# Optimization experiments

Hardware: AMD Instinct MI355X
Metric: run time of the kernel (lower is better)

Reference implementation:

```python
import jax, jax.numpy as jnp
import numpy as np

TEMP = 1.0  # routing_temperature

def _gelu(x):
    return jax.nn.gelu(x, approximate=False)  # torch nn.GELU default (erf)

def setup_inputs() -> dict:
    key = jax.random.key(0)
    ks = jax.random.split(key, 6)
    B, S, D, E, I = 8, 2048, 768, 8, 3072
    H = I // 2
    def xav(k, shape):
        fan_in, fan_out = shape[-2], shape[-1]
        lim = float(np.sqrt(6.0 / (fan_in + fan_out)))
        return jax.random.uniform(k, shape, jnp.float32, -lim, lim)
    return {
        "x":  jax.random.normal(ks[0], (B, S, D), jnp.float32),
        "Wr": xav(ks[1], (D, E)),
        "br": jnp.zeros((E,), jnp.float32),
        "W1": xav(ks[2], (E, D, I)), "b1": jnp.zeros((E, I), jnp.float32),
        "W2": xav(ks[3], (E, I, H)), "b2": jnp.zeros((E, H), jnp.float32),
        "W3": xav(ks[4], (E, H, D)), "b3": jnp.zeros((E, D), jnp.float32),
        "top_k": 2,
    }

def reference(x, Wr, br, W1, b1, W2, b2, W3, b3, top_k):
    B, S, D = x.shape
    E = Wr.shape[1]
    T = B * S
    xt = x.reshape(T, D)                              # flatten tokens
    logits = (xt @ Wr + br) / TEMP                    # [T, E]
    vals, sel = jax.lax.top_k(logits, top_k)          # [T, k]
    w = jax.nn.softmax(vals, axis=-1)                 # softmax over top-k scores
    # dense per-token combine weights (zero for unselected experts)
    combine = jnp.zeros((T, E), x.dtype).at[jnp.arange(T)[:, None], sel].add(w)
    def step(acc, p):
        W1e, b1e, W2e, b2e, W3e, b3e, ce = p
        h = _gelu(xt @ W1e + b1e)                     # [T, I]
        h = _gelu(h @ W2e + b2e)                      # [T, I//2]
        y = h @ W3e + b3e                             # [T, D]
        return acc + ce[:, None] * y, None
    acc0 = jnp.zeros((T, D), x.dtype)
    out, _ = jax.lax.scan(step, acc0, (W1, b1, W2, b2, W3, b3, combine.T))
    return out.reshape(B, S, D)
```

## Files before the change

kernel.cpp:

```cpp
#include <hip/hip_runtime.h>
#include <hip/hip_fp16.h>
#include <cstdint>
#include <cstddef>

#define TK 16384
#define DD 768
#define EE 8
#define II 3072
#define HH 1536

typedef _Float16 half8 __attribute__((ext_vector_type(8)));
typedef float floatx4 __attribute__((ext_vector_type(4)));

typedef const __attribute__((address_space(1))) uint32_t* gptr_t;
typedef __attribute__((address_space(3))) uint32_t* lptr_t;

#define GLOAD_LDS16(gp, lp) __builtin_amdgcn_global_load_lds( \
    (gptr_t)(const void*)(gp), (lptr_t)(void*)(lp), 16, 0, 0)

__device__ __forceinline__ void xcd_swizzle(int& e, int& m, int& n, bool rev) {
  int gx = gridDim.x, gy = gridDim.y;
  int f = (blockIdx.z * gy + blockIdx.y) * gx + blockIdx.x;
  if (rev) f = gx * gy * 8 - 1 - f;
  int xcd = f & 7, idx = f >> 3;
  int chunk = idx / gx, pos = idx - chunk * gx;
  int logical = chunk * (8 * gx) + xcd * gx + pos;
  int mn = gy * gx;
  e = logical / mn;
  int rem = logical - e * mn;
  m = rem / gx;
  n = rem - m * gx;
}

__global__ __launch_bounds__(256)
void cvtT_kernel(const float* __restrict__ in, __half* __restrict__ out,
                 int K, int N) {
  __shared__ float tile[64][65];
  int e = blockIdx.z;
  const float* inp = in + (size_t)e * K * N + (size_t)(blockIdx.y * 64) * N + blockIdx.x * 64;
  __half* outp = out + (size_t)e * K * N + (size_t)(blockIdx.x * 64) * K + blockIdx.y * 64;
  int s = threadIdx.x;
  int tx = s & 15, r0 = s >> 4;
#pragma unroll
  for (int i = 0; i < 4; ++i) {
    int k = r0 + i * 16;
    float4 v = *(const float4*)&inp[(size_t)k * N + tx * 4];
    tile[k][tx * 4 + 0] = v.x;
    tile[k][tx * 4 + 1] = v.y;
    tile[k][tx * 4 + 2] = v.z;
    tile[k][tx * 4 + 3] = v.w;
  }
  __syncthreads();
  int kp = s & 31;
#pragma unroll
  for (int i = 0; i < 8; ++i) {
    int n = (s >> 5) + i * 8;
    __half2 h = __floats2half2_rn(tile[2 * kp][n], tile[2 * kp + 1][n]);
    *(__half2*)&outp[(size_t)n * K + kp * 2] = h;
  }
}

__global__ __launch_bounds__(256)
void router_kernel(const float* __restrict__ x, const float* __restrict__ Wr,
                   const float* __restrict__ br, int* __restrict__ counts,
                   int* __restrict__ sel, float* __restrict__ wTok,
                   __half* __restrict__ xh) {
  __shared__ float wr_s[EE * DD];
  for (int i = threadIdx.x; i < EE * DD; i += 256) {
    int d = i >> 3, e = i & 7;
    wr_s[e * DD + d] = Wr[i];
  }
  __syncthreads();
  int wid = threadIdx.x >> 6, lane = threadIdx.x & 63;
  int t = blockIdx.x * 4 + wid;
  const float* xt = x + (size_t)t * DD;
  float acc[EE];
#pragma unroll
  for (int e = 0; e < EE; ++e) acc[e] = 0.f;
  for (int d = lane; d < DD; d += 64) {
    float xv = xt[d];
#pragma unroll
    for (int e = 0; e < EE; ++e) acc[e] += xv * wr_s[e * DD + d];
  }
#pragma unroll
  for (int off = 32; off > 0; off >>= 1)
#pragma unroll
    for (int e = 0; e < EE; ++e) acc[e] += __shfl_xor(acc[e], off);
  if (lane == 0) {
    float v[EE];
#pragma unroll
    for (int e = 0; e < EE; ++e) v[e] = acc[e] + br[e];
    int i0 = 0;
#pragma unroll
    for (int e = 1; e < EE; ++e) if (v[e] > v[i0]) i0 = e;
    int i1 = (i0 == 0) ? 1 : 0;
#pragma unroll
    for (int e = 0; e < EE; ++e) if (e != i0 && v[e] > v[i1] && e != i1) { if (v[e] > v[i1]) i1 = e; }
    float e1 = __expf(v[i1] - v[i0]);
    float s = 1.f / (1.f + e1);
    sel[2 * t] = i0; sel[2 * t + 1] = i1;
    wTok[2 * t] = s; wTok[2 * t + 1] = e1 * s;
    atomicAdd(&counts[i0], 1);
    atomicAdd(&counts[i1], 1);
  }
  const float4* xr = (const float4*)xt;
  uint2* xo = (uint2*)(xh + (size_t)t * DD);
#pragma unroll
  for (int j = 0; j < 3; ++j) {
    float4 v = xr[lane + j * 64];
    __half2 a = __floats2half2_rn(v.x, v.y);
    __half2 b = __floats2half2_rn(v.z, v.w);
    uint2 p;
    p.x = *(const unsigned int*)&a;
    p.y = *(const unsigned int*)&b;
    xo[lane + j * 64] = p;
  }
}

__global__ void offsets_kernel(const int* __restrict__ counts, int* __restrict__ offsets,
                               int* __restrict__ cursors) {
  if (threadIdx.x == 0) {
    int o = 0;
    for (int e = 0; e < EE; ++e) { offsets[e] = o; cursors[e] = o; o += counts[e]; }
  }
}

__global__ void scatter_kernel(const int* __restrict__ sel, int* __restrict__ cursors,
                               int* __restrict__ idxList, int* __restrict__ posTok) {
  int t = blockIdx.x * 256 + threadIdx.x;
  if (t < TK) {
#pragma unroll
    for (int k = 0; k < 2; ++k) {
      int e = sel[2 * t + k];
      int p = atomicAdd(&cursors[e], 1);
      idxList[p] = t;
      posTok[2 * t + k] = p;
    }
  }
}

template<int KD, int ND, bool GATHER, bool GELU, bool REV>
__device__ __forceinline__
void ffn_body(const __half* __restrict__ A, const __half* __restrict__ Wt,
              const float* __restrict__ Bias, __half* __restrict__ Out,
              const int* __restrict__ counts, const int* __restrict__ offsets,
              const int* __restrict__ idxList) {
  constexpr int NT = KD / 32;
  int e, mblk, nblk;
  xcd_swizzle(e, mblk, nblk, REV);
  const int cnt = counts[e];
  const int m0 = mblk * 256;
  if (cnt == 0 || m0 >= cnt) return;
  const int off = offsets[e];
  const int n0 = nblk * 256;
  const __half* We = Wt + (size_t)e * KD * ND;
  const float* be = Bias + (size_t)e * ND;

  __shared__ __align__(16) __half AsF[5 * 256 * 32];
  __shared__ __align__(16) __half BsF[4 * 256 * 32];

  const int tid = threadIdx.x;
  const int colh = (((tid & 3) ^ ((tid >> 3) & 3)) << 3);
  const __half* aptr2[2];
  const __half* bptr2[2];
#pragma unroll
  for (int i = 0; i < 2; ++i) {
    int r = i * 128 + (tid >> 2);
    int gr = m0 + r; if (gr > cnt - 1) gr = cnt - 1;
    size_t arow = GATHER ? (size_t)idxList[off + gr] : (size_t)(off + gr);
    aptr2[i] = A + arow * KD + colh;
    bptr2[i] = We + (size_t)(n0 + r) * KD + colh;
  }

#define STA(WOFF, TS) do { \
    GLOAD_LDS16(aptr2[0] + (TS) * 32, (char*)AsF + (WOFF) + tid * 16); \
    GLOAD_LDS16(aptr2[1] + (TS) * 32, (char*)AsF + (WOFF) + tid * 16 + 8192); } while (0)
#define STB(WOFF, TS) do { \
    GLOAD_LDS16(bptr2[0] + (TS) * 32, (char*)BsF + (WOFF) + tid * 16); \
    GLOAD_LDS16(bptr2[1] + (TS) * 32, (char*)BsF + (WOFF) + tid * 16 + 8192); } while (0)

  const int lane = tid & 63, wv = tid >> 6;
  const int wr = wv >> 2, wc = wv & 3;
  const int lrow = lane & 15, lg = lane >> 4;
  const int slotSwz = lg ^ ((lrow >> 1) & 3);
  const int aBase = (wr * 128 + lrow) * 64 + slotSwz * 16;
  const int bBase = (wc * 64 + lrow) * 64 + slotSwz * 16;

  floatx4 acc[8][4];
#pragma unroll
  for (int mi = 0; mi < 8; ++mi)
#pragma unroll
    for (int ni = 0; ni < 4; ++ni) acc[mi][ni] = (floatx4){0.f, 0.f, 0.f, 0.f};

  STA(0 * 16384, 0);
  STB(0 * 16384, 0);
  STA(1 * 16384, 1);
  STB(1 * 16384, 1);
  STA(2 * 16384, 2);
  STB(2 * 16384, 2);
  STA(3 * 16384, 3);
  asm volatile("s_waitcnt vmcnt(10)" ::: "memory");
  __builtin_amdgcn_s_barrier();
  __builtin_amdgcn_sched_barrier(0);

  int rA = 0, wA = 4 * 16384;
  int rB = 0, wB = 3 * 16384;

#pragma unroll 1
  for (int t = 0; t < NT; ++t) {
    half8 af[8], bf[4];
#pragma unroll
    for (int mi = 0; mi < 8; ++mi)
      af[mi] = *(const half8*)((const char*)AsF + rA + aBase + mi * 1024);
#pragma unroll
    for (int ni = 0; ni < 4; ++ni)
      bf[ni] = *(const half8*)((const char*)BsF + rB + bBase + ni * 1024);
    if (t + 3 < NT) STB(wB, t + 3);
    if (t + 4 < NT) STA(wA, t + 4);
    __builtin_amdgcn_s_setprio(1);
#pragma unroll
    for (int mi = 0; mi < 8; ++mi)
#pragma unroll
      for (int ni = 0; ni < 4; ++ni)
        acc[mi][ni] = __builtin_amdgcn_mfma_f32_16x16x32_f16(
            af[mi], bf[ni], acc[mi][ni], 0, 0, 0);
    __builtin_amdgcn_s_setprio(0);
    if (t + 4 < NT) { asm volatile("s_waitcnt vmcnt(10)" ::: "memory"); }
    else            { asm volatile("s_waitcnt vmcnt(0)"  ::: "memory"); }
    __builtin_amdgcn_s_barrier();
    __builtin_amdgcn_sched_barrier(0);
    rA += 16384; if (rA == 5 * 16384) rA = 0;
    wA += 16384; if (wA == 5 * 16384) wA = 0;
    rB += 16384; if (rB == 4 * 16384) rB = 0;
    wB += 16384; if (wB == 4 * 16384) wB = 0;
  }

  const int crow = m0 + wr * 128 + lg * 4;
  const int ccol = n0 + wc * 64 + lrow;
  float bv[4];
#pragma unroll
  for (int ni = 0; ni < 4; ++ni) bv[ni] = be[ccol + ni * 16];
#pragma unroll
  for (int mi = 0; mi < 8; ++mi) {
#pragma unroll
    for (int j = 0; j < 4; ++j) {
      int r = crow + mi * 16 + j;
      if (r < cnt) {
#pragma unroll
        for (int ni = 0; ni < 4; ++ni) {
          float v = acc[mi][ni][j] + bv[ni];
          if (GELU) v = 0.5f * v * (1.f + erff(v * 0.70710678118654752f));
          Out[(size_t)(off + r) * ND + ccol + ni * 16] = __float2half(v);
        }
      }
    }
  }
#undef STA
#undef STB
}

__global__ __launch_bounds__(512, 1)
void ffn_s1(const __half* __restrict__ A, const __half* __restrict__ Wt,
            const float* __restrict__ Bias, __half* __restrict__ Out,
            const int* __restrict__ counts, const int* __restrict__ offsets,
            const int* __restrict__ idxL) {
  ffn_body<DD, II, true, true, false>(A, Wt, Bias, Out, counts, offsets, idxL);
}
__global__ __launch_bounds__(512, 1)
void ffn_s2(const __half* __restrict__ A, const __half* __restrict__ Wt,
            const float* __restrict__ Bias, __half* __restrict__ Out,
            const int* __restrict__ counts, const int* __restrict__ offsets,
            const int* __restrict__ idxL) {
  ffn_body<II, HH, false, true, true>(A, Wt, Bias, Out, counts, offsets, idxL);
}
__global__ __launch_bounds__(512, 1)
void ffn_s3(const __half* __restrict__ A, const __half* __restrict__ Wt,
            const float* __restrict__ Bias, __half* __restrict__ Out,
            const int* __restrict__ counts, const int* __restrict__ offsets,
            const int* __restrict__ idxL) {
  ffn_body<HH, DD, false, false, false>(A, Wt, Bias, Out, counts, offsets, idxL);
}

__global__ void combine_kernel(const __half* __restrict__ yc, const float* __restrict__ wTok,
                               const int* __restrict__ posTok, float* __restrict__ out) {
  int t = blockIdx.x;
  int d = threadIdx.x * 4;
  if (d >= DD) return;
  float w0 = wTok[2 * t], w1 = wTok[2 * t + 1];
  const __half2* a = (const __half2*)(yc + (size_t)posTok[2 * t] * DD + d);
  const __half2* b = (const __half2*)(yc + (size_t)posTok[2 * t + 1] * DD + d);
  float2 a0 = __half22float2(a[0]), a1 = __half22float2(a[1]);
  float2 b0 = __half22float2(b[0]), b1 = __half22float2(b[1]);
  float4 r;
  r.x = w0 * a0.x + w1 * b0.x;
  r.y = w0 * a0.y + w1 * b0.y;
  r.z = w0 * a1.x + w1 * b1.x;
  r.w = w0 * a1.y + w1 * b1.y;
  *(float4*)(out + (size_t)t * DD + d) = r;
}

extern "C" void kernel_launch(void* const* d_in, const int* in_sizes, int n_in,
                              void* d_out, int out_size, void* d_ws, size_t ws_size,
                              hipStream_t stream) {
  const float* x  = (const float*)d_in[0];
  const float* Wr = (const float*)d_in[1];
  const float* br = (const float*)d_in[2];
  const float* W1 = (const float*)d_in[3];
  const float* b1 = (const float*)d_in[4];
  const float* W2 = (const float*)d_in[5];
  const float* b2 = (const float*)d_in[6];
  const float* W3 = (const float*)d_in[7];
  const float* b3 = (const float*)d_in[8];
  float* out = (float*)d_out;

  char* ws = (char*)d_ws;
  size_t o = 0;
  auto alloc = [&](size_t bytes) {
    char* p = ws + o;
    o += (bytes + 255) & ~(size_t)255;
    return p;
  };
  __half* xh   = (__half*)alloc((size_t)TK * DD * 2);
  __half* w1t  = (__half*)alloc((size_t)EE * DD * II * 2);
  __half* w2t  = (__half*)alloc((size_t)EE * II * HH * 2);
  __half* w3t  = (__half*)alloc((size_t)EE * HH * DD * 2);
  __half* h1   = (__half*)alloc((size_t)2 * TK * II * 2);
  __half* h2   = (__half*)alloc((size_t)2 * TK * HH * 2);
  __half* yc   = (__half*)alloc((size_t)2 * TK * DD * 2);
  int*   idxL  = (int*)alloc(2 * TK * 4);
  int*   sel   = (int*)alloc(2 * TK * 4);
  float* wTok  = (float*)alloc(2 * TK * 4);
  int*   posT  = (int*)alloc(2 * TK * 4);
  int*   counts  = (int*)alloc(256);
  int*   offsets = (int*)alloc(256);
  int*   cursors = (int*)alloc(256);
  if (o > ws_size) return;

  hipMemsetAsync(counts, 0, 256, stream);

  cvtT_kernel<<<dim3(II / 64, DD / 64, EE), 256, 0, stream>>>(W1, w1t, DD, II);
  cvtT_kernel<<<dim3(HH / 64, II / 64, EE), 256, 0, stream>>>(W2, w2t, II, HH);
  cvtT_kernel<<<dim3(DD / 64, HH / 64, EE), 256, 0, stream>>>(W3, w3t, HH, DD);
  router_kernel<<<TK / 4, 256, 0, stream>>>(x, Wr, br, counts, sel, wTok, xh);
  offsets_kernel<<<1, 64, 0, stream>>>(counts, offsets, cursors);
  scatter_kernel<<<TK / 256, 256, 0, stream>>>(sel, cursors, idxL, posT);

  ffn_s1<<<dim3(II / 256, 64, EE), 512, 0, stream>>>(xh, w1t, b1, h1, counts, offsets, idxL);
  ffn_s2<<<dim3(HH / 256, 64, EE), 512, 0, stream>>>(h1, w2t, b2, h2, counts, offsets, idxL);
  ffn_s3<<<dim3(DD / 256, 64, EE), 512, 0, stream>>>(h2, w3t, b3, yc, counts, offsets, idxL);

  combine_kernel<<<TK, 192, 0, stream>>>(yc, wTok, posT, out);
}
```

Before: 1.470 ms.

## Use 128x128 tiles with 256-thread blocks for first and third FFN GEMMs

Adds a smaller-tile GEMM variant (128x128 output tile, 4 waves, triple-buffered LDS, two blocks per CU) and uses it for the first and third expert FFN stages. The middle stage keeps the 256x256 tile kernel. The goal is better CU occupancy and less tail waste on the narrower GEMMs, where 256x256 tiles yield few blocks per expert. In exchange, each operand load is reused less, which raises global and L2 traffic per FLOP.

```diff
diff --git a/kernel.cpp b/kernel.cpp
--- a/kernel.cpp
+++ b/kernel.cpp
@@ -141,10 +141,10 @@
 
 template<int KD, int ND, bool GATHER, bool GELU, bool REV>
 __device__ __forceinline__
-void ffn_body(const __half* __restrict__ A, const __half* __restrict__ Wt,
-              const float* __restrict__ Bias, __half* __restrict__ Out,
-              const int* __restrict__ counts, const int* __restrict__ offsets,
-              const int* __restrict__ idxList) {
+void ffn_body_big(const __half* __restrict__ A, const __half* __restrict__ Wt,
+                  const float* __restrict__ Bias, __half* __restrict__ Out,
+                  const int* __restrict__ counts, const int* __restrict__ offsets,
+                  const int* __restrict__ idxList) {
   constexpr int NT = KD / 32;
   int e, mblk, nblk;
   xcd_swizzle(e, mblk, nblk, REV);
@@ -259,26 +259,139 @@
 #undef STB
 }
 
-__global__ __launch_bounds__(512, 1)
+template<int KD, int ND, bool GATHER, bool GELU, bool REV>
+__device__ __forceinline__
+void ffn_body_small(const __half* __restrict__ A, const __half* __restrict__ Wt,
+                    const float* __restrict__ Bias, __half* __restrict__ Out,
+                    const int* __restrict__ counts, const int* __restrict__ offsets,
+                    const int* __restrict__ idxList) {
+  constexpr int NT = KD / 32;
+  int e, mblk, nblk;
+  xcd_swizzle(e, mblk, nblk, REV);
+  const int cnt = counts[e];
+  const int m0 = mblk * 128;
+  if (cnt == 0 || m0 >= cnt) return;
+  const int off = offsets[e];
+  const int n0 = nblk * 128;
+  const __half* We = Wt + (size_t)e * KD * ND;
+  const float* be = Bias + (size_t)e * ND;
+
+  __shared__ __align__(16) __half AsF[3 * 128 * 32];
+  __shared__ __align__(16) __half BsF[3 * 128 * 32];
+
+  const int tid = threadIdx.x;
+  const int colh = (((tid & 3) ^ ((tid >> 3) & 3)) << 3);
+  const __half* aptr2[2];
+  const __half* bptr2[2];
+#pragma unroll
+  for (int i = 0; i < 2; ++i) {
+    int r = i * 64 + (tid >> 2);
+    int gr = m0 + r; if (gr > cnt - 1) gr = cnt - 1;
+    size_t arow = GATHER ? (size_t)idxList[off + gr] : (size_t)(off + gr);
+    aptr2[i] = A + arow * KD + colh;
+    bptr2[i] = We + (size_t)(n0 + r) * KD + colh;
+  }
+
+#define STA(WOFF, TS) do { \
+    GLOAD_LDS16(aptr2[0] + (TS) * 32, (char*)AsF + (WOFF) + tid * 16); \
+    GLOAD_LDS16(aptr2[1] + (TS) * 32, (char*)AsF + (WOFF) + tid * 16 + 4096); } while (0)
+#define STB(WOFF, TS) do { \
+    GLOAD_LDS16(bptr2[0] + (TS) * 32, (char*)BsF + (WOFF) + tid * 16); \
+    GLOAD_LDS16(bptr2[1] + (TS) * 32, (char*)BsF + (WOFF) + tid * 16 + 4096); } while (0)
+
+  const int lane = tid & 63, wv = tid >> 6;
+  const int wr = wv >> 1, wc = wv & 1;
+  const int lrow = lane & 15, lg = lane >> 4;
+  const int slotSwz = lg ^ ((lrow >> 1) & 3);
+  const int aBase = (wr * 64 + lrow) * 64 + slotSwz * 16;
+  const int bBase = (wc * 64 + lrow) * 64 + slotSwz * 16;
+
+  floatx4 acc[4][4];
+#pragma unroll
+  for (int mi = 0; mi < 4; ++mi)
+#pragma unroll
+    for (int ni = 0; ni < 4; ++ni) acc[mi][ni] = (floatx4){0.f, 0.f, 0.f, 0.f};
+
+  STB(0, 0);
+  STA(0, 0);
+  STB(8192, 1);
+  STA(8192, 1);
+  asm volatile("s_waitcnt vmcnt(4)" ::: "memory");
+  __builtin_amdgcn_s_barrier();
+  __builtin_amdgcn_sched_barrier(0);
+
+  int rBuf = 0, wBuf = 2 * 8192;
+
+#pragma unroll 1
+  for (int t = 0; t < NT; ++t) {
+    half8 af[4], bf[4];
+#pragma unroll
+    for (int mi = 0; mi < 4; ++mi)
+      af[mi] = *(const half8*)((const char*)AsF + rBuf + aBase + mi * 1024);
+#pragma unroll
+    for (int ni = 0; ni < 4; ++ni)
+      bf[ni] = *(const half8*)((const char*)BsF + rBuf + bBase + ni * 1024);
+    if (t + 2 < NT) { STB(wBuf, t + 2); STA(wBuf, t + 2); }
+    __builtin_amdgcn_s_setprio(1);
+#pragma unroll
+    for (int mi = 0; mi < 4; ++mi)
+#pragma unroll
+      for (int ni = 0; ni < 4; ++ni)
+        acc[mi][ni] = __builtin_amdgcn_mfma_f32_16x16x32_f16(
+            af[mi], bf[ni], acc[mi][ni], 0, 0, 0);
+    __builtin_amdgcn_s_setprio(0);
+    if (t + 2 < NT) { asm volatile("s_waitcnt vmcnt(4)" ::: "memory"); }
+    else            { asm volatile("s_waitcnt vmcnt(0)" ::: "memory"); }
+    __builtin_amdgcn_s_barrier();
+    __builtin_amdgcn_sched_barrier(0);
+    rBuf += 8192; if (rBuf == 3 * 8192) rBuf = 0;
+    wBuf += 8192; if (wBuf == 3 * 8192) wBuf = 0;
+  }
+
+  const int crow = m0 + wr * 64 + lg * 4;
+  const int ccol = n0 + wc * 64 + lrow;
+  float bv[4];
+#pragma unroll
+  for (int ni = 0; ni < 4; ++ni) bv[ni] = be[ccol + ni * 16];
+#pragma unroll
+  for (int mi = 0; mi < 4; ++mi) {
+#pragma unroll
+    for (int j = 0; j < 4; ++j) {
+      int r = crow + mi * 16 + j;
+      if (r < cnt) {
+#pragma unroll
+        for (int ni = 0; ni < 4; ++ni) {
+          float v = acc[mi][ni][j] + bv[ni];
+          if (GELU) v = 0.5f * v * (1.f + erff(v * 0.70710678118654752f));
+          Out[(size_t)(off + r) * ND + ccol + ni * 16] = __float2half(v);
+        }
+      }
+    }
+  }
+#undef STA
+#undef STB
+}
+
+__global__ __launch_bounds__(256, 2)
 void ffn_s1(const __half* __restrict__ A, const __half* __restrict__ Wt,
             const float* __restrict__ Bias, __half* __restrict__ Out,
             const int* __restrict__ counts, const int* __restrict__ offsets,
             const int* __restrict__ idxL) {
-  ffn_body<DD, II, true, true, false>(A, Wt, Bias, Out, counts, offsets, idxL);
+  ffn_body_small<DD, II, true, true, false>(A, Wt, Bias, Out, counts, offsets, idxL);
 }
 __global__ __launch_bounds__(512, 1)
 void ffn_s2(const __half* __restrict__ A, const __half* __restrict__ Wt,
             const float* __restrict__ Bias, __half* __restrict__ Out,
             const int* __restrict__ counts, const int* __restrict__ offsets,
             const int* __restrict__ idxL) {
-  ffn_body<II, HH, false, true, true>(A, Wt, Bias, Out, counts, offsets, idxL);
-}
-__global__ __launch_bounds__(512, 1)
+  ffn_body_big<II, HH, false, true, true>(A, Wt, Bias, Out, counts, offsets, idxL);
+}
+__global__ __launch_bounds__(256, 2)
 void ffn_s3(const __half* __restrict__ A, const __half* __restrict__ Wt,
             const float* __restrict__ Bias, __half* __restrict__ Out,
             const int* __restrict__ counts, const int* __restrict__ offsets,
             const int* __restrict__ idxL) {
-  ffn_body<HH, DD, false, false, false>(A, Wt, Bias, Out, counts, offsets, idxL);
+  ffn_body_small<HH, DD, false, false, false>(A, Wt, Bias, Out, counts, offsets, idxL);
 }
 
 __global__ void combine_kernel(const __half* __restrict__ yc, const float* __restrict__ wTok,
@@ -345,9 +458,9 @@
   offsets_kernel<<<1, 64, 0, stream>>>(counts, offsets, cursors);
   scatter_kernel<<<TK / 256, 256, 0, stream>>>(sel, cursors, idxL, posT);
 
-  ffn_s1<<<dim3(II / 256, 64, EE), 512, 0, stream>>>(xh, w1t, b1, h1, counts, offsets, idxL);
+  ffn_s1<<<dim3(II / 128, 128, EE), 256, 0, stream>>>(xh, w1t, b1, h1, counts, offsets, idxL);
   ffn_s2<<<dim3(HH / 256, 64, EE), 512, 0, stream>>>(h1, w2t, b2, h2, counts, offsets, idxL);
-  ffn_s3<<<dim3(DD / 256, 64, EE), 512, 0, stream>>>(h2, w3t, b3, yc, counts, offsets, idxL);
+  ffn_s3<<<dim3(DD / 128, 128, EE), 256, 0, stream>>>(h2, w3t, b3, yc, counts, offsets, idxL);
 
   combine_kernel<<<TK, 192, 0, stream>>>(yc, wTok, posT, out);
 }
```

After: 1.425 ms (median of 3 runs). 1.03x faster.
